# Kernel tuning notes

Measured on AMD Instinct MI355X. Metric: run time of the kernel, lower is better.

The kernel has to match this reference:

```python
import jax, jax.numpy as jnp
import numpy as np

N, E = 100000, 1600000
IN, HID, NCLS = 128, 128, 64


def setup_inputs() -> dict:
    key = jax.random.key(0)
    ks = jax.random.split(key, 8)
    x = jax.random.normal(ks[0], (N, IN), jnp.float32)
    edge_index = jax.random.randint(ks[1], (2, E), 0, N, dtype=jnp.int32)
    s1 = 1.0 / np.sqrt(IN)
    s2 = 1.0 / np.sqrt(HID)
    return {
        "x": x,
        "edge_index": edge_index,
        "Wl1": jax.random.uniform(ks[2], (IN, HID), jnp.float32, -s1, s1),
        "Wr1": jax.random.uniform(ks[3], (IN, HID), jnp.float32, -s1, s1),
        "b1": jnp.zeros((HID,), jnp.float32),
        "Wl2": jax.random.uniform(ks[4], (HID, NCLS), jnp.float32, -s2, s2),
        "Wr2": jax.random.uniform(ks[5], (HID, NCLS), jnp.float32, -s2, s2),
        "b2": jnp.zeros((NCLS,), jnp.float32),
    }


def _sage_conv(x, src, dst, inv_deg, Wl, Wr, b):
    # mean-aggregate neighbor features at each destination node (PyG SAGEConv)
    agg = jax.ops.segment_sum(x[src], dst, num_segments=N)  # [N, d]
    agg = agg * inv_deg[:, None]
    # out = lin_l(mean_j x_j) + lin_r(x_i); bias lives in lin_l
    return agg @ Wl + x @ Wr + b


def reference(x, edge_index, Wl1, Wr1, b1, Wl2, Wr2, b2):
    src, dst = edge_index[0], edge_index[1]
    deg = jax.ops.segment_sum(jnp.ones((E,), jnp.float32), dst, num_segments=N)
    inv_deg = 1.0 / jnp.maximum(deg, 1.0)
    h = _sage_conv(x, src, dst, inv_deg, Wl1, Wr1, b1)
    h = jax.nn.relu(h)
    # dropout is identity at inference (training=False)
    h = _sage_conv(h, src, dst, inv_deg, Wl2, Wr2, b2)
    return jax.nn.log_softmax(h, axis=1)
```

## Files before the change

### kernel.cpp

```cpp
#include <hip/hip_runtime.h>
#include <hip/hip_bf16.h>


typedef __attribute__((ext_vector_type(8))) short short8;
typedef __attribute__((ext_vector_type(4))) float f32x4;
typedef __attribute__((ext_vector_type(2))) float f32x2;

#define NPB 512
#define BCAP 16384
#define CHUNK 8192

__device__ __forceinline__ ushort f2bf(float f) {
    unsigned u = __float_as_uint(f);
    return (ushort)((u + 0x7fff + ((u >> 16) & 1)) >> 16);
}
__device__ __forceinline__ float bflo(unsigned v) { return __uint_as_float(v << 16); }
__device__ __forceinline__ float bfhi(unsigned v) { return __uint_as_float(v & 0xffff0000u); }
__device__ __forceinline__ unsigned pk4bf(float a, float b) {
    return (unsigned)f2bf(a) | ((unsigned)f2bf(b) << 16);
}
__device__ __forceinline__ f32x2 shflx2(f32x2 v, int m) {
    f32x2 r; r[0] = __shfl_xor(v[0], m); r[1] = __shfl_xor(v[1], m); return r;
}

__device__ __forceinline__ void wfrag_one(const float* W, ushort* Wf, int i, int COLS) {
    int j = i & 7, m = (i >> 3) & 15, kc = (i >> 7) & 15, ct = i >> 11;
    Wf[i] = f2bf(W[(kc * 8 + j) * COLS + ct * 16 + m]);
}

__global__ void __launch_bounds__(256)
k1_scatter_cvtw(const int* __restrict__ src, const int* __restrict__ dst,
                int* __restrict__ bcount, unsigned* __restrict__ bbuf, int E, int NSC,
                const float* __restrict__ Wl1, const float* __restrict__ Wr1,
                const float* __restrict__ Wl2, const float* __restrict__ Wr2,
                ushort* __restrict__ Wf_l1, ushort* __restrict__ Wf_r1,
                ushort* __restrict__ Wf_l2, ushort* __restrict__ Wf_r2) {
    int tid = threadIdx.x;
    if ((int)blockIdx.x >= NSC) {
        int i = ((int)blockIdx.x - NSC) * 256 + tid;
        if (i < 16384)       wfrag_one(Wl1, Wf_l1, i, 128);
        else if (i < 32768)  wfrag_one(Wr1, Wf_r1, i - 16384, 128);
        else if (i < 40960)  wfrag_one(Wl2, Wf_l2, i - 32768, 64);
        else if (i < 49152)  wfrag_one(Wr2, Wf_r2, i - 40960, 64);
        return;
    }
    __shared__ unsigned entry[CHUNK];
    __shared__ unsigned char ebkt[CHUNK];
    __shared__ int lhist[256], lbase[256], lcur[256];
    lhist[tid] = 0;
    __syncthreads();
    int e0 = blockIdx.x * CHUNK;
    int cnt = min(CHUNK, E - e0);
    int nv = cnt >> 2;
    for (int t = tid; t < nv; t += 256) {
        int4 d4 = ((const int4*)(dst + e0))[t];
        int4 s4 = ((const int4*)(src + e0))[t];
        int i = t * 4;
        int b0 = d4.x >> 9, b1 = d4.y >> 9, b2 = d4.z >> 9, b3 = d4.w >> 9;
        entry[i + 0] = ((unsigned)s4.x << 9) | (unsigned)(d4.x & 511);
        entry[i + 1] = ((unsigned)s4.y << 9) | (unsigned)(d4.y & 511);
        entry[i + 2] = ((unsigned)s4.z << 9) | (unsigned)(d4.z & 511);
        entry[i + 3] = ((unsigned)s4.w << 9) | (unsigned)(d4.w & 511);
        ebkt[i + 0] = (unsigned char)b0; ebkt[i + 1] = (unsigned char)b1;
        ebkt[i + 2] = (unsigned char)b2; ebkt[i + 3] = (unsigned char)b3;
        atomicAdd(&lhist[b0], 1); atomicAdd(&lhist[b1], 1);
        atomicAdd(&lhist[b2], 1); atomicAdd(&lhist[b3], 1);
    }
    for (int i = (nv << 2) + tid; i < cnt; i += 256) {
        int d = dst[e0 + i], s = src[e0 + i];
        int b = d >> 9;
        entry[i] = ((unsigned)s << 9) | (unsigned)(d & 511);
        ebkt[i] = (unsigned char)b;
        atomicAdd(&lhist[b], 1);
    }
    __syncthreads();
    int h = lhist[tid];
    lbase[tid] = (h > 0) ? atomicAdd(&bcount[tid], h) : 0;
    lcur[tid] = 0;
    __syncthreads();
    for (int i = tid; i < cnt; i += 256) {
        int b = ebkt[i];
        int o = atomicAdd(&lcur[b], 1);
        bbuf[(long)b * BCAP + lbase[b] + o] = entry[i];
    }
}

template <int CTOT>
__device__ __forceinline__ void stage_weights(const ushort* __restrict__ Wfl,
                                              const ushort* __restrict__ Wfr,
                                              ushort* dst, int tid) {
    constexpr int HALF = CTOT / 2;
    constexpr int ITERS = (CTOT * 2) / 8192;
#pragma unroll
    for (int r = 0; r < ITERS; ++r) {
        int u = r * 4096 + tid * 8;
        const ushort* s = (u < HALF) ? (Wfl + u) : (Wfr + (u - HALF));
        *(short8*)(dst + u) = *(const short8*)s;
    }
}

template <int COLS, bool F32IN>
__device__ __forceinline__ void proj_body(int bid, int tid,
                            const void* __restrict__ xin,
                            const ushort* __restrict__ Wfl, const ushort* __restrict__ Wfr,
                            const float* __restrict__ bias,
                            unsigned char* __restrict__ p8, ushort* __restrict__ q, int N,
                            ushort* wsm) {
    constexpr int CT = COLS / 16;
    stage_weights<2 * COLS * 128>(Wfl, Wfr, wsm, tid);
    __syncthreads();
    const ushort* Wl = wsm;
    const ushort* Wr = wsm + COLS * 128;

    int wave = tid >> 6, lane = tid & 63;
    int quad = lane >> 4, m = lane & 15;
    long row0 = (long)bid * 128 + wave * 16;
    long node = row0 + m;
    long arow = (node < N) ? node : (N - 1);

    f32x4 accp[CT], accq[CT];
#pragma unroll
    for (int ct = 0; ct < CT; ++ct) { accp[ct] = (f32x4)0.0f; accq[ct] = (f32x4)0.0f; }

#pragma unroll
    for (int kk = 0; kk < 128; kk += 32) {
        short8 b;
        if (F32IN) {
            const float* xf = (const float*)xin + arow * 128 + kk + quad * 8;
            float4 f0 = *(const float4*)xf;
            float4 f1 = *(const float4*)(xf + 4);
            b[0] = (short)f2bf(f0.x); b[1] = (short)f2bf(f0.y);
            b[2] = (short)f2bf(f0.z); b[3] = (short)f2bf(f0.w);
            b[4] = (short)f2bf(f1.x); b[5] = (short)f2bf(f1.y);
            b[6] = (short)f2bf(f1.z); b[7] = (short)f2bf(f1.w);
        } else {
            b = *(const short8*)((const ushort*)xin + arow * 128 + kk + quad * 8);
        }
        int kc = (kk >> 3) + quad;
#pragma unroll
        for (int ct = 0; ct < CT; ++ct) {
            int boff = ((ct * 16 + kc) * 16 + m) * 8;
            short8 al = *(const short8*)(Wl + boff);
            short8 ar = *(const short8*)(Wr + boff);
            accp[ct] = __builtin_amdgcn_mfma_f32_16x16x32_bf16(al, b, accp[ct], 0, 0, 0);
            accq[ct] = __builtin_amdgcn_mfma_f32_16x16x32_bf16(ar, b, accq[ct], 0, 0, 0);
        }
    }

    if (node < N) {
#pragma unroll
        for (int ct = 0; ct < CT; ++ct) {
            int c0 = ct * 16 + quad * 4;
            float4 bv = *(const float4*)(bias + c0);
            float q0 = accq[ct][0] + bv.x, q1 = accq[ct][1] + bv.y;
            float q2 = accq[ct][2] + bv.z, q3 = accq[ct][3] + bv.w;
            unsigned w = (unsigned)__builtin_amdgcn_cvt_pk_fp8_f32(accp[ct][0], accp[ct][1], 0, false);
            w = (unsigned)__builtin_amdgcn_cvt_pk_fp8_f32(accp[ct][2], accp[ct][3], (int)w, true);
            *(unsigned*)(p8 + node * COLS + c0) = w;
            uint2 qw; qw.x = pk4bf(q0, q1); qw.y = pk4bf(q2, q3);
            *(uint2*)(q + node * COLS + c0) = qw;
        }
    }
}

__global__ void __launch_bounds__(512, 4)
k2_csr_proj1(const unsigned* __restrict__ bbuf, const int* __restrict__ bcount,
             int* __restrict__ row_start, int* __restrict__ degw,
             float* __restrict__ inv_deg, int* __restrict__ ssrc, int NBcsr, int N,
             const float* __restrict__ x,
             const ushort* __restrict__ Wfl, const ushort* __restrict__ Wfr,
             const float* __restrict__ bias,
             unsigned char* __restrict__ p8, ushort* __restrict__ q) {
    extern __shared__ char smem[];
    int tid = threadIdx.x;
    if ((int)blockIdx.x >= NBcsr) {
        proj_body<128, true>((int)blockIdx.x - NBcsr, tid, x, Wfl, Wfr, bias, p8, q, N,
                             (ushort*)smem);
        return;
    }
    int* sdeg = (int*)smem;
    int* lcur = sdeg + NPB;
    int* wsum = lcur + NPB;
    int b = blockIdx.x;
    int node0 = b * NPB;
    sdeg[tid] = 0;
    __syncthreads();
    int cnt = bcount[b];
    long base = (long)b * BCAP;
    const unsigned* bb = bbuf + base;
    int nv = cnt >> 2;
    for (int t = tid; t < nv; t += 512) {
        uint4 e = ((const uint4*)bb)[t];
        atomicAdd(&sdeg[e.x & 511], 1);
        atomicAdd(&sdeg[e.y & 511], 1);
        atomicAdd(&sdeg[e.z & 511], 1);
        atomicAdd(&sdeg[e.w & 511], 1);
    }
    for (int i = (nv << 2) + tid; i < cnt; i += 512)
        atomicAdd(&sdeg[bb[i] & 511], 1);
    __syncthreads();
    int lane = tid & 63, wv = tid >> 6;
    int c0 = sdeg[tid];
    int v = c0;
#pragma unroll
    for (int o = 1; o < 64; o <<= 1) {
        int t = __shfl_up(v, o);
        if (lane >= o) v += t;
    }
    if (lane == 63) wsum[wv] = v;
    __syncthreads();
    int add = 0;
    for (int w = 0; w < wv; ++w) add += wsum[w];
    int rs0 = v + add - c0;
    lcur[tid] = rs0;
    if (node0 + tid < N) {
        row_start[node0 + tid] = (int)(base + rs0);
        degw[node0 + tid] = c0;
        inv_deg[node0 + tid] = 1.0f / (float)(c0 > 1 ? c0 : 1);
    }
    __syncthreads();
    for (int t = tid; t < nv; t += 512) {
        uint4 e = ((const uint4*)bb)[t];
        int p0 = atomicAdd(&lcur[e.x & 511], 1);
        int p1 = atomicAdd(&lcur[e.y & 511], 1);
        int p2 = atomicAdd(&lcur[e.z & 511], 1);
        int p3 = atomicAdd(&lcur[e.w & 511], 1);
        ssrc[base + p0] = (int)(e.x >> 9);
        ssrc[base + p1] = (int)(e.y >> 9);
        ssrc[base + p2] = (int)(e.z >> 9);
        ssrc[base + p3] = (int)(e.w >> 9);
    }
    for (int i = (nv << 2) + tid; i < cnt; i += 512) {
        unsigned w = bb[i];
        int pos = atomicAdd(&lcur[w & 511], 1);
        ssrc[base + pos] = (int)(w >> 9);
    }
}

__global__ void __launch_bounds__(256)
agg_relu_kernel(const unsigned char* __restrict__ p8,
                const ushort* __restrict__ q,
                const int* __restrict__ ssrc,
                const int* __restrict__ row_start,
                const int* __restrict__ deg,
                const float* __restrict__ inv_deg,
                ushort* __restrict__ hb, int N) {
    int wave = threadIdx.x >> 6, lane = threadIdx.x & 63;
    int n = blockIdx.x * 4 + wave;
    if (n >= N) return;
    int g = lane >> 4, lm = lane & 15;
    int start = row_start[n], d = deg[n];
    const int* sp = ssrc + start;
    const unsigned char* pb = p8 + lm * 8;
    f32x2 a0 = (f32x2)0.f, a1 = (f32x2)0.f, a2 = (f32x2)0.f, a3 = (f32x2)0.f;
    int j = 0;
    for (; j + 16 <= d; j += 16) {
        int s0 = sp[j + g], s1 = sp[j + 4 + g], s2 = sp[j + 8 + g], s3 = sp[j + 12 + g];
        uint2 v0 = *(const uint2*)(pb + (long)s0 * 128);
        uint2 v1 = *(const uint2*)(pb + (long)s1 * 128);
        uint2 v2 = *(const uint2*)(pb + (long)s2 * 128);
        uint2 v3 = *(const uint2*)(pb + (long)s3 * 128);
#pragma unroll
        for (int t = 0; t < 4; ++t) {
            uint2 vv = (t == 0) ? v0 : (t == 1) ? v1 : (t == 2) ? v2 : v3;
            a0 += __builtin_amdgcn_cvt_pk_f32_fp8((int)vv.x, false);
            a1 += __builtin_amdgcn_cvt_pk_f32_fp8((int)vv.x, true);
            a2 += __builtin_amdgcn_cvt_pk_f32_fp8((int)vv.y, false);
            a3 += __builtin_amdgcn_cvt_pk_f32_fp8((int)vv.y, true);
        }
    }
    for (; j < d; j += 4) {
        int idx = j + g;
        int s = sp[idx < d ? idx : j];
        uint2 vv = *(const uint2*)(pb + (long)s * 128);
        if (idx < d) {
            a0 += __builtin_amdgcn_cvt_pk_f32_fp8((int)vv.x, false);
            a1 += __builtin_amdgcn_cvt_pk_f32_fp8((int)vv.x, true);
            a2 += __builtin_amdgcn_cvt_pk_f32_fp8((int)vv.y, false);
            a3 += __builtin_amdgcn_cvt_pk_f32_fp8((int)vv.y, true);
        }
    }
    a0 += shflx2(a0, 16); a1 += shflx2(a1, 16);
    a2 += shflx2(a2, 16); a3 += shflx2(a3, 16);
    a0 += shflx2(a0, 32); a1 += shflx2(a1, 32);
    a2 += shflx2(a2, 32); a3 += shflx2(a3, 32);
    if (g == 0) {
        float iv = inv_deg[n];
        uint4 qv = *(const uint4*)(q + (long)n * 128 + lm * 8);
        float h0 = fmaxf(a0[0] * iv + bflo(qv.x), 0.f);
        float h1 = fmaxf(a0[1] * iv + bfhi(qv.x), 0.f);
        float h2 = fmaxf(a1[0] * iv + bflo(qv.y), 0.f);
        float h3 = fmaxf(a1[1] * iv + bfhi(qv.y), 0.f);
        float h4 = fmaxf(a2[0] * iv + bflo(qv.z), 0.f);
        float h5 = fmaxf(a2[1] * iv + bfhi(qv.z), 0.f);
        float h6 = fmaxf(a3[0] * iv + bflo(qv.w), 0.f);
        float h7 = fmaxf(a3[1] * iv + bfhi(qv.w), 0.f);
        uint4 hw;
        hw.x = pk4bf(h0, h1); hw.y = pk4bf(h2, h3);
        hw.z = pk4bf(h4, h5); hw.w = pk4bf(h6, h7);
        *(uint4*)(hb + (long)n * 128 + lm * 8) = hw;
    }
}

__global__ void __launch_bounds__(512, 4)
proj2_kernel(const ushort* __restrict__ hb,
             const ushort* __restrict__ Wfl, const ushort* __restrict__ Wfr,
             const float* __restrict__ bias,
             unsigned char* __restrict__ u8, ushort* __restrict__ v, int N) {
    __shared__ ushort wsm[2 * 64 * 128];
    proj_body<64, false>((int)blockIdx.x, (int)threadIdx.x, hb, Wfl, Wfr, bias, u8, v, N,
                         wsm);
}

__global__ void __launch_bounds__(256)
agg_lsm_kernel(const unsigned char* __restrict__ u8,
               const ushort* __restrict__ v,
               const int* __restrict__ ssrc,
               const int* __restrict__ row_start,
               const int* __restrict__ deg,
               const float* __restrict__ inv_deg,
               float* __restrict__ out, int N) {
    int wave = threadIdx.x >> 6, lane = threadIdx.x & 63;
    int n = blockIdx.x * 4 + wave;
    if (n >= N) return;
    int g = lane >> 3, lm = lane & 7;
    int start = row_start[n], d = deg[n];
    const int* sp = ssrc + start;
    const unsigned char* ub = u8 + lm * 8;
    f32x2 a0 = (f32x2)0.f, a1 = (f32x2)0.f, a2 = (f32x2)0.f, a3 = (f32x2)0.f;
    int j = 0;
    for (; j + 16 <= d; j += 16) {
        int s0 = sp[j + g], s1 = sp[j + 8 + g];
        uint2 v0 = *(const uint2*)(ub + (long)s0 * 64);
        uint2 v1 = *(const uint2*)(ub + (long)s1 * 64);
#pragma unroll
        for (int t = 0; t < 2; ++t) {
            uint2 vv = (t == 0) ? v0 : v1;
            a0 += __builtin_amdgcn_cvt_pk_f32_fp8((int)vv.x, false);
            a1 += __builtin_amdgcn_cvt_pk_f32_fp8((int)vv.x, true);
            a2 += __builtin_amdgcn_cvt_pk_f32_fp8((int)vv.y, false);
            a3 += __builtin_amdgcn_cvt_pk_f32_fp8((int)vv.y, true);
        }
    }
    for (; j < d; j += 8) {
        int idx = j + g;
        int s = sp[idx < d ? idx : j];
        uint2 vv = *(const uint2*)(ub + (long)s * 64);
        if (idx < d) {
            a0 += __builtin_amdgcn_cvt_pk_f32_fp8((int)vv.x, false);
            a1 += __builtin_amdgcn_cvt_pk_f32_fp8((int)vv.x, true);
            a2 += __builtin_amdgcn_cvt_pk_f32_fp8((int)vv.y, false);
            a3 += __builtin_amdgcn_cvt_pk_f32_fp8((int)vv.y, true);
        }
    }
    a0 += shflx2(a0, 8);  a1 += shflx2(a1, 8);  a2 += shflx2(a2, 8);  a3 += shflx2(a3, 8);
    a0 += shflx2(a0, 16); a1 += shflx2(a1, 16); a2 += shflx2(a2, 16); a3 += shflx2(a3, 16);
    a0 += shflx2(a0, 32); a1 += shflx2(a1, 32); a2 += shflx2(a2, 32); a3 += shflx2(a3, 32);

    float iv = inv_deg[n];
    uint4 vv = *(const uint4*)(v + (long)n * 64 + lm * 8);
    float z0 = a0[0] * iv + bflo(vv.x), z1 = a0[1] * iv + bfhi(vv.x);
    float z2 = a1[0] * iv + bflo(vv.y), z3 = a1[1] * iv + bfhi(vv.y);
    float z4 = a2[0] * iv + bflo(vv.z), z5 = a2[1] * iv + bfhi(vv.z);
    float z6 = a3[0] * iv + bflo(vv.w), z7 = a3[1] * iv + bfhi(vv.w);
    float mx = fmaxf(fmaxf(fmaxf(z0, z1), fmaxf(z2, z3)),
                     fmaxf(fmaxf(z4, z5), fmaxf(z6, z7)));
#pragma unroll
    for (int o = 4; o > 0; o >>= 1) mx = fmaxf(mx, __shfl_xor(mx, o));
    float e = (__expf(z0 - mx) + __expf(z1 - mx)) + (__expf(z2 - mx) + __expf(z3 - mx)) +
              (__expf(z4 - mx) + __expf(z5 - mx)) + (__expf(z6 - mx) + __expf(z7 - mx));
#pragma unroll
    for (int o = 4; o > 0; o >>= 1) e += __shfl_xor(e, o);
    float ls = mx + __logf(e);
    if (g == 0) {
        float4 o0, o1;
        o0.x = z0 - ls; o0.y = z1 - ls; o0.z = z2 - ls; o0.w = z3 - ls;
        o1.x = z4 - ls; o1.y = z5 - ls; o1.z = z6 - ls; o1.w = z7 - ls;
        *(float4*)(out + (long)n * 64 + lm * 8) = o0;
        *(float4*)(out + (long)n * 64 + lm * 8 + 4) = o1;
    }
}

extern "C" void kernel_launch(void* const* d_in, const int* in_sizes, int n_in,
                              void* d_out, int out_size, void* d_ws, size_t ws_size,
                              hipStream_t stream) {
    const float* x   = (const float*)d_in[0];
    const int*   ei  = (const int*)d_in[1];
    const float* Wl1 = (const float*)d_in[2];
    const float* Wr1 = (const float*)d_in[3];
    const float* b1  = (const float*)d_in[4];
    const float* Wl2 = (const float*)d_in[5];
    const float* Wr2 = (const float*)d_in[6];
    const float* b2  = (const float*)d_in[7];

    const int N = in_sizes[0] / 128;
    const int E = in_sizes[1] / 2;
    const int* src = ei;
    const int* dst = ei + E;
    const int NB = (N + NPB - 1) / NPB;
    const int NSC = (E + CHUNK - 1) / CHUNK;

    size_t off = 0;
    auto take = [&](size_t nbytes) -> void* {
        void* ptr = (void*)((char*)d_ws + off);
        off += (nbytes + 255) & ~(size_t)255;
        return ptr;
    };
    int*      bcount    = (int*)take((size_t)NB * 4);
    unsigned* bbuf      = (unsigned*)take((size_t)NB * BCAP * 4);
    int*      row_start = (int*)take((size_t)N * 4);
    int*      degw      = (int*)take((size_t)N * 4);
    float*    inv_deg   = (float*)take((size_t)N * 4);
    int*      ssrc      = (int*)take((size_t)NB * BCAP * 4);
    unsigned char* p8   = (unsigned char*)take((size_t)N * 128);
    ushort*   q         = (ushort*)take((size_t)N * 128 * 2);
    ushort*   hb        = (ushort*)take((size_t)N * 128 * 2);
    ushort*   Wf_l1     = (ushort*)take(128 * 128 * 2);
    ushort*   Wf_r1     = (ushort*)take(128 * 128 * 2);
    ushort*   Wf_l2     = (ushort*)take(64 * 128 * 2);
    ushort*   Wf_r2     = (ushort*)take(64 * 128 * 2);
    unsigned char* u8 = p8;
    ushort*        v  = q;
    (void)ws_size; (void)n_in; (void)out_size;

    static bool attr_set = false;
    if (!attr_set) {
        hipFuncSetAttribute((const void*)k2_csr_proj1,
                            hipFuncAttributeMaxDynamicSharedMemorySize, 65536);
        attr_set = true;
    }

    hipMemsetAsync(bcount, 0, (size_t)NB * 4, stream);

    k1_scatter_cvtw<<<NSC + 192, 256, 0, stream>>>(src, dst, bcount, bbuf, E, NSC,
                                                   Wl1, Wr1, Wl2, Wr2,
                                                   Wf_l1, Wf_r1, Wf_l2, Wf_r2);

    int P1 = (N + 127) / 128;
    k2_csr_proj1<<<NB + P1, 512, 65536, stream>>>(bbuf, bcount, row_start, degw, inv_deg,
                                                  ssrc, NB, N, x, Wf_l1, Wf_r1, b1, p8, q);

    agg_relu_kernel<<<(N + 3) / 4, 256, 0, stream>>>(p8, q, ssrc, row_start, degw, inv_deg, hb, N);

    proj2_kernel<<<(N + 127) / 128, 512, 0, stream>>>(hb, Wf_l2, Wf_r2, b2, u8, v, N);
    agg_lsm_kernel<<<(N + 3) / 4, 256, 0, stream>>>(u8, v, ssrc, row_start, degw, inv_deg,
                                                    (float*)d_out, N);
}
```

Measured before the change: 260.4 us.

## Remap aggregation lanes to 4-byte fp8 gathers and pack row_start/degree

```diff
diff --git a/kernel.cpp b/kernel.cpp
--- a/kernel.cpp
+++ b/kernel.cpp
@@ -17,7 +17,9 @@
 __device__ __forceinline__ float bflo(unsigned v) { return __uint_as_float(v << 16); }
 __device__ __forceinline__ float bfhi(unsigned v) { return __uint_as_float(v & 0xffff0000u); }
 __device__ __forceinline__ unsigned pk4bf(float a, float b) {
-    return (unsigned)f2bf(a) | ((unsigned)f2bf(b) << 16);
+    unsigned r;
+    asm("v_cvt_pk_bf16_f32 %0, %1, %2" : "=v"(r) : "v"(a), "v"(b));
+    return r;
 }
 __device__ __forceinline__ f32x2 shflx2(f32x2 v, int m) {
     f32x2 r; r[0] = __shfl_xor(v[0], m); r[1] = __shfl_xor(v[1], m); return r;
@@ -129,10 +131,12 @@
             const float* xf = (const float*)xin + arow * 128 + kk + quad * 8;
             float4 f0 = *(const float4*)xf;
             float4 f1 = *(const float4*)(xf + 4);
-            b[0] = (short)f2bf(f0.x); b[1] = (short)f2bf(f0.y);
-            b[2] = (short)f2bf(f0.z); b[3] = (short)f2bf(f0.w);
-            b[4] = (short)f2bf(f1.x); b[5] = (short)f2bf(f1.y);
-            b[6] = (short)f2bf(f1.z); b[7] = (short)f2bf(f1.w);
+            union { short8 s; unsigned u[4]; } bu;
+            bu.u[0] = pk4bf(f0.x, f0.y);
+            bu.u[1] = pk4bf(f0.z, f0.w);
+            bu.u[2] = pk4bf(f1.x, f1.y);
+            bu.u[3] = pk4bf(f1.z, f1.w);
+            b = bu.s;
         } else {
             b = *(const short8*)((const ushort*)xin + arow * 128 + kk + quad * 8);
         }
@@ -165,7 +169,7 @@
 
 __global__ void __launch_bounds__(512, 4)
 k2_csr_proj1(const unsigned* __restrict__ bbuf, const int* __restrict__ bcount,
-             int* __restrict__ row_start, int* __restrict__ degw,
+             int* __restrict__ rsd,
              float* __restrict__ inv_deg, int* __restrict__ ssrc, int NBcsr, int N,
              const float* __restrict__ x,
              const ushort* __restrict__ Wfl, const ushort* __restrict__ Wfr,
@@ -214,8 +218,8 @@
     int rs0 = v + add - c0;
     lcur[tid] = rs0;
     if (node0 + tid < N) {
-        row_start[node0 + tid] = (int)(base + rs0);
-        degw[node0 + tid] = c0;
+        int2 rv; rv.x = (int)(base + rs0); rv.y = c0;
+        *(int2*)(rsd + 2 * (node0 + tid)) = rv;
         inv_deg[node0 + tid] = 1.0f / (float)(c0 > 1 ? c0 : 1);
     }
     __syncthreads();
@@ -241,64 +245,94 @@
 agg_relu_kernel(const unsigned char* __restrict__ p8,
                 const ushort* __restrict__ q,
                 const int* __restrict__ ssrc,
-                const int* __restrict__ row_start,
-                const int* __restrict__ deg,
+                const int* __restrict__ rsd,
                 const float* __restrict__ inv_deg,
                 ushort* __restrict__ hb, int N) {
     int wave = threadIdx.x >> 6, lane = threadIdx.x & 63;
     int n = blockIdx.x * 4 + wave;
     if (n >= N) return;
-    int g = lane >> 4, lm = lane & 15;
-    int start = row_start[n], d = deg[n];
+    int g = lane >> 5, lm = lane & 31;
+    int2 rv = *(const int2*)(rsd + 2 * n);
+    int start = rv.x, d = rv.y;
+    float iv = inv_deg[n];
+    uint2 qv = make_uint2(0u, 0u);
+    if (g == 0) qv = *(const uint2*)(q + (long)n * 128 + lm * 4);
     const int* sp = ssrc + start;
-    const unsigned char* pb = p8 + lm * 8;
-    f32x2 a0 = (f32x2)0.f, a1 = (f32x2)0.f, a2 = (f32x2)0.f, a3 = (f32x2)0.f;
+    const unsigned char* pb = p8 + lm * 4;
+    f32x2 a0 = (f32x2)0.f, a1 = (f32x2)0.f;
     int j = 0;
     for (; j + 16 <= d; j += 16) {
-        int s0 = sp[j + g], s1 = sp[j + 4 + g], s2 = sp[j + 8 + g], s3 = sp[j + 12 + g];
-        uint2 v0 = *(const uint2*)(pb + (long)s0 * 128);
-        uint2 v1 = *(const uint2*)(pb + (long)s1 * 128);
-        uint2 v2 = *(const uint2*)(pb + (long)s2 * 128);
-        uint2 v3 = *(const uint2*)(pb + (long)s3 * 128);
-#pragma unroll
-        for (int t = 0; t < 4; ++t) {
-            uint2 vv = (t == 0) ? v0 : (t == 1) ? v1 : (t == 2) ? v2 : v3;
-            a0 += __builtin_amdgcn_cvt_pk_f32_fp8((int)vv.x, false);
-            a1 += __builtin_amdgcn_cvt_pk_f32_fp8((int)vv.x, true);
-            a2 += __builtin_amdgcn_cvt_pk_f32_fp8((int)vv.y, false);
-            a3 += __builtin_amdgcn_cvt_pk_f32_fp8((int)vv.y, true);
-        }
-    }
-    for (; j < d; j += 4) {
+        int s0 = sp[j + g],      s1 = sp[j + 2 + g],  s2 = sp[j + 4 + g],  s3 = sp[j + 6 + g];
+        int s4 = sp[j + 8 + g],  s5 = sp[j + 10 + g], s6 = sp[j + 12 + g], s7 = sp[j + 14 + g];
+        unsigned v0 = *(const unsigned*)(pb + (long)s0 * 128);
+        unsigned v1 = *(const unsigned*)(pb + (long)s1 * 128);
+        unsigned v2 = *(const unsigned*)(pb + (long)s2 * 128);
+        unsigned v3 = *(const unsigned*)(pb + (long)s3 * 128);
+        unsigned v4 = *(const unsigned*)(pb + (long)s4 * 128);
+        unsigned v5 = *(const unsigned*)(pb + (long)s5 * 128);
+        unsigned v6 = *(const unsigned*)(pb + (long)s6 * 128);
+        unsigned v7 = *(const unsigned*)(pb + (long)s7 * 128);
+        a0 += __builtin_amdgcn_cvt_pk_f32_fp8((int)v0, false);
+        a1 += __builtin_amdgcn_cvt_pk_f32_fp8((int)v0, true);
+        a0 += __builtin_amdgcn_cvt_pk_f32_fp8((int)v1, false);
+        a1 += __builtin_amdgcn_cvt_pk_f32_fp8((int)v1, true);
+        a0 += __builtin_amdgcn_cvt_pk_f32_fp8((int)v2, false);
+        a1 += __builtin_amdgcn_cvt_pk_f32_fp8((int)v2, true);
+        a0 += __builtin_amdgcn_cvt_pk_f32_fp8((int)v3, false);
+        a1 += __builtin_amdgcn_cvt_pk_f32_fp8((int)v3, true);
+        a0 += __builtin_amdgcn_cvt_pk_f32_fp8((int)v4, false);
+        a1 += __builtin_amdgcn_cvt_pk_f32_fp8((int)v4, true);
+        a0 += __builtin_amdgcn_cvt_pk_f32_fp8((int)v5, false);
+        a1 += __builtin_amdgcn_cvt_pk_f32_fp8((int)v5, true);
+        a0 += __builtin_amdgcn_cvt_pk_f32_fp8((int)v6, false);
+        a1 += __builtin_amdgcn_cvt_pk_f32_fp8((int)v6, true);
+        a0 += __builtin_amdgcn_cvt_pk_f32_fp8((int)v7, false);
+        a1 += __builtin_amdgcn_cvt_pk_f32_fp8((int)v7, true);
+    }
+    if (j + 8 <= d) {
+        int s0 = sp[j + g], s1 = sp[j + 2 + g], s2 = sp[j + 4 + g], s3 = sp[j + 6 + g];
+        unsigned v0 = *(const unsigned*)(pb + (long)s0 * 128);
+        unsigned v1 = *(const unsigned*)(pb + (long)s1 * 128);
+        unsigned v2 = *(const unsigned*)(pb + (long)s2 * 128);
+        unsigned v3 = *(const unsigned*)(pb + (long)s3 * 128);
+        a0 += __builtin_amdgcn_cvt_pk_f32_fp8((int)v0, false);
+        a1 += __builtin_amdgcn_cvt_pk_f32_fp8((int)v0, true);
+        a0 += __builtin_amdgcn_cvt_pk_f32_fp8((int)v1, false);
+        a1 += __builtin_amdgcn_cvt_pk_f32_fp8((int)v1, true);
+        a0 += __builtin_amdgcn_cvt_pk_f32_fp8((int)v2, false);
+        a1 += __builtin_amdgcn_cvt_pk_f32_fp8((int)v2, true);
+        a0 += __builtin_amdgcn_cvt_pk_f32_fp8((int)v3, false);
+        a1 += __builtin_amdgcn_cvt_pk_f32_fp8((int)v3, true);
+        j += 8;
+    }
+    if (j + 4 <= d) {
+        int s0 = sp[j + g], s1 = sp[j + 2 + g];
+        unsigned v0 = *(const unsigned*)(pb + (long)s0 * 128);
+        unsigned v1 = *(const unsigned*)(pb + (long)s1 * 128);
+        a0 += __builtin_amdgcn_cvt_pk_f32_fp8((int)v0, false);
+        a1 += __builtin_amdgcn_cvt_pk_f32_fp8((int)v0, true);
+        a0 += __builtin_amdgcn_cvt_pk_f32_fp8((int)v1, false);
+        a1 += __builtin_amdgcn_cvt_pk_f32_fp8((int)v1, true);
+        j += 4;
+    }
+    for (; j < d; j += 2) {
         int idx = j + g;
         int s = sp[idx < d ? idx : j];
-        uint2 vv = *(const uint2*)(pb + (long)s * 128);
+        unsigned vv = *(const unsigned*)(pb + (long)s * 128);
         if (idx < d) {
-            a0 += __builtin_amdgcn_cvt_pk_f32_fp8((int)vv.x, false);
-            a1 += __builtin_amdgcn_cvt_pk_f32_fp8((int)vv.x, true);
-            a2 += __builtin_amdgcn_cvt_pk_f32_fp8((int)vv.y, false);
-            a3 += __builtin_amdgcn_cvt_pk_f32_fp8((int)vv.y, true);
+            a0 += __builtin_amdgcn_cvt_pk_f32_fp8((int)vv, false);
+            a1 += __builtin_amdgcn_cvt_pk_f32_fp8((int)vv, true);
         }
     }
-    a0 += shflx2(a0, 16); a1 += shflx2(a1, 16);
-    a2 += shflx2(a2, 16); a3 += shflx2(a3, 16);
     a0 += shflx2(a0, 32); a1 += shflx2(a1, 32);
-    a2 += shflx2(a2, 32); a3 += shflx2(a3, 32);
     if (g == 0) {
-        float iv = inv_deg[n];
-        uint4 qv = *(const uint4*)(q + (long)n * 128 + lm * 8);
         float h0 = fmaxf(a0[0] * iv + bflo(qv.x), 0.f);
         float h1 = fmaxf(a0[1] * iv + bfhi(qv.x), 0.f);
         float h2 = fmaxf(a1[0] * iv + bflo(qv.y), 0.f);
         float h3 = fmaxf(a1[1] * iv + bfhi(qv.y), 0.f);
-        float h4 = fmaxf(a2[0] * iv + bflo(qv.z), 0.f);
-        float h5 = fmaxf(a2[1] * iv + bfhi(qv.z), 0.f);
-        float h6 = fmaxf(a3[0] * iv + bflo(qv.w), 0.f);
-        float h7 = fmaxf(a3[1] * iv + bfhi(qv.w), 0.f);
-        uint4 hw;
+        uint2 hw;
         hw.x = pk4bf(h0, h1); hw.y = pk4bf(h2, h3);
-        hw.z = pk4bf(h4, h5); hw.w = pk4bf(h6, h7);
-        *(uint4*)(hb + (long)n * 128 + lm * 8) = hw;
+        *(uint2*)(hb + (long)n * 128 + lm * 4) = hw;
     }
 }
 
@@ -316,68 +350,71 @@
 agg_lsm_kernel(const unsigned char* __restrict__ u8,
                const ushort* __restrict__ v,
                const int* __restrict__ ssrc,
-               const int* __restrict__ row_start,
-               const int* __restrict__ deg,
+               const int* __restrict__ rsd,
                const float* __restrict__ inv_deg,
                float* __restrict__ out, int N) {
     int wave = threadIdx.x >> 6, lane = threadIdx.x & 63;
     int n = blockIdx.x * 4 + wave;
     if (n >= N) return;
-    int g = lane >> 3, lm = lane & 7;
-    int start = row_start[n], d = deg[n];
+    int g = lane >> 4, lm = lane & 15;
+    int2 rv = *(const int2*)(rsd + 2 * n);
+    int start = rv.x, d = rv.y;
+    float iv = inv_deg[n];
+    uint2 vv2 = *(const uint2*)(v + (long)n * 64 + lm * 4);
     const int* sp = ssrc + start;
-    const unsigned char* ub = u8 + lm * 8;
-    f32x2 a0 = (f32x2)0.f, a1 = (f32x2)0.f, a2 = (f32x2)0.f, a3 = (f32x2)0.f;
+    const unsigned char* ub = u8 + lm * 4;
+    f32x2 a0 = (f32x2)0.f, a1 = (f32x2)0.f;
     int j = 0;
     for (; j + 16 <= d; j += 16) {
-        int s0 = sp[j + g], s1 = sp[j + 8 + g];
-        uint2 v0 = *(const uint2*)(ub + (long)s0 * 64);
-        uint2 v1 = *(const uint2*)(ub + (long)s1 * 64);
-#pragma unroll
-        for (int t = 0; t < 2; ++t) {
-            uint2 vv = (t == 0) ? v0 : v1;
-            a0 += __builtin_amdgcn_cvt_pk_f32_fp8((int)vv.x, false);
-            a1 += __builtin_amdgcn_cvt_pk_f32_fp8((int)vv.x, true);
-            a2 += __builtin_amdgcn_cvt_pk_f32_fp8((int)vv.y, false);
-            a3 += __builtin_amdgcn_cvt_pk_f32_fp8((int)vv.y, true);
-        }
-    }
-    for (; j < d; j += 8) {
+        int s0 = sp[j + g], s1 = sp[j + 4 + g], s2 = sp[j + 8 + g], s3 = sp[j + 12 + g];
+        unsigned v0 = *(const unsigned*)(ub + (long)s0 * 64);
+        unsigned v1 = *(const unsigned*)(ub + (long)s1 * 64);
+        unsigned v2 = *(const unsigned*)(ub + (long)s2 * 64);
+        unsigned v3 = *(const unsigned*)(ub + (long)s3 * 64);
+        a0 += __builtin_amdgcn_cvt_pk_f32_fp8((int)v0, false);
+        a1 += __builtin_amdgcn_cvt_pk_f32_fp8((int)v0, true);
+        a0 += __builtin_amdgcn_cvt_pk_f32_fp8((int)v1, false);
+        a1 += __builtin_amdgcn_cvt_pk_f32_fp8((int)v1, true);
+        a0 += __builtin_amdgcn_cvt_pk_f32_fp8((int)v2, false);
+        a1 += __builtin_amdgcn_cvt_pk_f32_fp8((int)v2, true);
+        a0 += __builtin_amdgcn_cvt_pk_f32_fp8((int)v3, false);
+        a1 += __builtin_amdgcn_cvt_pk_f32_fp8((int)v3, true);
+    }
+    if (j + 8 <= d) {
+        int s0 = sp[j + g], s1 = sp[j + 4 + g];
+        unsigned v0 = *(const unsigned*)(ub + (long)s0 * 64);
+        unsigned v1 = *(const unsigned*)(ub + (long)s1 * 64);
+        a0 += __builtin_amdgcn_cvt_pk_f32_fp8((int)v0, false);
+        a1 += __builtin_amdgcn_cvt_pk_f32_fp8((int)v0, true);
+        a0 += __builtin_amdgcn_cvt_pk_f32_fp8((int)v1, false);
+        a1 += __builtin_amdgcn_cvt_pk_f32_fp8((int)v1, true);
+        j += 8;
+    }
+    for (; j < d; j += 4) {
         int idx = j + g;
         int s = sp[idx < d ? idx : j];
-        uint2 vv = *(const uint2*)(ub + (long)s * 64);
+        unsigned vv = *(const unsigned*)(ub + (long)s * 64);
         if (idx < d) {
-            a0 += __builtin_amdgcn_cvt_pk_f32_fp8((int)vv.x, false);
-            a1 += __builtin_amdgcn_cvt_pk_f32_fp8((int)vv.x, true);
-            a2 += __builtin_amdgcn_cvt_pk_f32_fp8((int)vv.y, false);
-            a3 += __builtin_amdgcn_cvt_pk_f32_fp8((int)vv.y, true);
+            a0 += __builtin_amdgcn_cvt_pk_f32_fp8((int)vv, false);
+            a1 += __builtin_amdgcn_cvt_pk_f32_fp8((int)vv, true);
         }
     }
-    a0 += shflx2(a0, 8);  a1 += shflx2(a1, 8);  a2 += shflx2(a2, 8);  a3 += shflx2(a3, 8);
-    a0 += shflx2(a0, 16); a1 += shflx2(a1, 16); a2 += shflx2(a2, 16); a3 += shflx2(a3, 16);
-    a0 += shflx2(a0, 32); a1 += shflx2(a1, 32); a2 += shflx2(a2, 32); a3 += shflx2(a3, 32);
-
-    float iv = inv_deg[n];
-    uint4 vv = *(const uint4*)(v + (long)n * 64 + lm * 8);
-    float z0 = a0[0] * iv + bflo(vv.x), z1 = a0[1] * iv + bfhi(vv.x);
-    float z2 = a1[0] * iv + bflo(vv.y), z3 = a1[1] * iv + bfhi(vv.y);
-    float z4 = a2[0] * iv + bflo(vv.z), z5 = a2[1] * iv + bfhi(vv.z);
-    float z6 = a3[0] * iv + bflo(vv.w), z7 = a3[1] * iv + bfhi(vv.w);
-    float mx = fmaxf(fmaxf(fmaxf(z0, z1), fmaxf(z2, z3)),
-                     fmaxf(fmaxf(z4, z5), fmaxf(z6, z7)));
-#pragma unroll
-    for (int o = 4; o > 0; o >>= 1) mx = fmaxf(mx, __shfl_xor(mx, o));
-    float e = (__expf(z0 - mx) + __expf(z1 - mx)) + (__expf(z2 - mx) + __expf(z3 - mx)) +
-              (__expf(z4 - mx) + __expf(z5 - mx)) + (__expf(z6 - mx) + __expf(z7 - mx));
-#pragma unroll
-    for (int o = 4; o > 0; o >>= 1) e += __shfl_xor(e, o);
+    a0 += shflx2(a0, 16); a1 += shflx2(a1, 16);
+    a0 += shflx2(a0, 32); a1 += shflx2(a1, 32);
+
+    float z0 = a0[0] * iv + bflo(vv2.x), z1 = a0[1] * iv + bfhi(vv2.x);
+    float z2 = a1[0] * iv + bflo(vv2.y), z3 = a1[1] * iv + bfhi(vv2.y);
+    float mx = fmaxf(fmaxf(z0, z1), fmaxf(z2, z3));
+#pragma unroll
+    for (int o = 8; o > 0; o >>= 1) mx = fmaxf(mx, __shfl_xor(mx, o));
+    float e = (__expf(z0 - mx) + __expf(z1 - mx)) + (__expf(z2 - mx) + __expf(z3 - mx));
+#pragma unroll
+    for (int o = 8; o > 0; o >>= 1) e += __shfl_xor(e, o);
     float ls = mx + __logf(e);
     if (g == 0) {
-        float4 o0, o1;
+        float4 o0;
         o0.x = z0 - ls; o0.y = z1 - ls; o0.z = z2 - ls; o0.w = z3 - ls;
-        o1.x = z4 - ls; o1.y = z5 - ls; o1.z = z6 - ls; o1.w = z7 - ls;
-        *(float4*)(out + (long)n * 64 + lm * 8) = o0;
-        *(float4*)(out + (long)n * 64 + lm * 8 + 4) = o1;
+        *(float4*)(out + (long)n * 64 + lm * 4) = o0;
     }
 }
 
@@ -408,8 +445,7 @@
     };
     int*      bcount    = (int*)take((size_t)NB * 4);
     unsigned* bbuf      = (unsigned*)take((size_t)NB * BCAP * 4);
-    int*      row_start = (int*)take((size_t)N * 4);
-    int*      degw      = (int*)take((size_t)N * 4);
+    int*      rsd       = (int*)take((size_t)N * 8);
     float*    inv_deg   = (float*)take((size_t)N * 4);
     int*      ssrc      = (int*)take((size_t)NB * BCAP * 4);
     unsigned char* p8   = (unsigned char*)take((size_t)N * 128);
@@ -437,12 +473,12 @@
                                                    Wf_l1, Wf_r1, Wf_l2, Wf_r2);
 
     int P1 = (N + 127) / 128;
-    k2_csr_proj1<<<NB + P1, 512, 65536, stream>>>(bbuf, bcount, row_start, degw, inv_deg,
+    k2_csr_proj1<<<NB + P1, 512, 65536, stream>>>(bbuf, bcount, rsd, inv_deg,
                                                   ssrc, NB, N, x, Wf_l1, Wf_r1, b1, p8, q);
 
-    agg_relu_kernel<<<(N + 3) / 4, 256, 0, stream>>>(p8, q, ssrc, row_start, degw, inv_deg, hb, N);
+    agg_relu_kernel<<<(N + 3) / 4, 256, 0, stream>>>(p8, q, ssrc, rsd, inv_deg, hb, N);
 
     proj2_kernel<<<(N + 127) / 128, 512, 0, stream>>>(hb, Wf_l2, Wf_r2, b2, u8, v, N);
-    agg_lsm_kernel<<<(N + 3) / 4, 256, 0, stream>>>(u8, v, ssrc, row_start, degw, inv_deg,
+    agg_lsm_kernel<<<(N + 3) / 4, 256, 0, stream>>>(u8, v, ssrc, rsd, inv_deg,
                                                     (float*)d_out, N);
 }
```

Result: faster. 251.9 us (-3.3%).
